# Optimization experiments

Measured on AMD Instinct MI355X. Metric: run time of the kernel, lower is better.

The kernel has to match this reference:

```python
import jax, jax.numpy as jnp
import numpy as np

E = 1_000_000
C_IN = 11
H = 64
N_LAYERS = 4
LN_EPS = 1e-5


def setup_inputs() -> dict:
    key = jax.random.key(0)
    ks = jax.random.split(key, 12)
    x = jax.random.normal(ks[0], (E, C_IN), dtype=jnp.float32)
    neighbors = jax.random.randint(ks[1], (E, 4), 0, E)
    s0 = 1.0 / np.sqrt(5 * C_IN)
    s1 = 1.0 / np.sqrt(5 * H)
    w0 = jax.random.uniform(ks[2], (5 * C_IN, H), jnp.float32, -s0, s0)
    b0 = jax.random.uniform(ks[3], (H,), jnp.float32, -s0, s0)
    w_rest = jax.random.uniform(ks[4], (N_LAYERS - 1, 5 * H, H), jnp.float32, -s1, s1)
    b_rest = jax.random.uniform(ks[5], (N_LAYERS - 1, H), jnp.float32, -s1, s1)
    ln_g = jnp.ones((N_LAYERS, H), jnp.float32)
    ln_b = jnp.zeros((N_LAYERS, H), jnp.float32)
    sc1 = 1.0 / np.sqrt(H)
    sc2 = 1.0 / np.sqrt(H // 2)
    cw1 = jax.random.uniform(ks[6], (H, H // 2), jnp.float32, -sc1, sc1)
    cb1 = jax.random.uniform(ks[7], (H // 2,), jnp.float32, -sc1, sc1)
    cw2 = jax.random.uniform(ks[8], (H // 2, 1), jnp.float32, -sc2, sc2)
    cb2 = jax.random.uniform(ks[9], (1,), jnp.float32, -sc2, sc2)
    return {"x": x, "neighbors": neighbors, "w0": w0, "b0": b0,
            "w_rest": w_rest, "b_rest": b_rest, "ln_g": ln_g, "ln_b": ln_b,
            "cw1": cw1, "cb1": cb1, "cw2": cw2, "cb2": cb2}


def _mesh_conv(x, neighbors, W, b):
    # Gather 4-ring neighbor features: [E,4,C]
    n = x[neighbors]
    a, bb, c, d = n[:, 0], n[:, 1], n[:, 2], n[:, 3]
    # Symmetric MeshCNN features -> 5*C, then linear projection.
    feats = jnp.concatenate([x, jnp.abs(a - c), a + c, jnp.abs(bb - d), bb + d], axis=-1)
    return feats @ W + b


def _layernorm(h, g, b):
    mu = jnp.mean(h, axis=-1, keepdims=True)
    var = jnp.var(h, axis=-1, keepdims=True)
    return (h - mu) * jax.lax.rsqrt(var + LN_EPS) * g + b


def reference(x, neighbors, w0, b0, w_rest, b_rest, ln_g, ln_b, cw1, cb1, cw2, cb2):
    # Layer 0 (no residual; dropout is identity in eval mode)
    h = jax.nn.relu(_layernorm(_mesh_conv(x, neighbors, w0, b0), ln_g[0], ln_b[0]))
    x = h
    for i in range(1, N_LAYERS):
        h = _mesh_conv(x, neighbors, w_rest[i - 1], b_rest[i - 1])
        h = jax.nn.relu(_layernorm(h, ln_g[i], ln_b[i]))
        x = h + x  # residual from layer 2 onward (shapes match)
    z = jax.nn.relu(x @ cw1 + cb1)
    logits = (z @ cw2 + cb2).squeeze(-1)
    return logits
```

## Files before the change

### kernel.cpp

```cpp
#include <hip/hip_runtime.h>
#include <hip/hip_bf16.h>
#include <math.h>

#define E_EDGES 1000000
#define LN_EPS  1e-5f

typedef unsigned short u16;
typedef __bf16 bf16x8 __attribute__((ext_vector_type(8)));
typedef float  f32x16 __attribute__((ext_vector_type(16)));

__device__ __forceinline__ float lo2f(unsigned d) {
    union { unsigned u; float f; } v; v.u = d << 16; return v.f;
}
__device__ __forceinline__ float hi2f(unsigned d) {
    union { unsigned u; float f; } v; v.u = d & 0xffff0000u; return v.f;
}
__device__ __forceinline__ unsigned pk2(float lo, float hi) {
    __hip_bfloat162 h = __float22bfloat162_rn(make_float2(lo, hi));
    unsigned r; __builtin_memcpy(&r, &h, 4); return r;
}

__global__ __launch_bounds__(256) void wconv_kernel(
    const float* __restrict__ wr, const float* __restrict__ w0,
    u16* __restrict__ wf)
{
    const int s = blockIdx.x * 256 + threadIdx.x;
    const int l    = s & 63;
    const int nt   = (s >> 6) & 1;
    const int col  = nt * 32 + (l & 31);
    const int half = l >> 5;
    uint4 pk;
    if (s < 3 * 2560) {
        const int L  = s / 2560;
        const int sl = s % 2560;
        const int kb = (sl >> 7) * 16 + half * 8;
        const float* W = wr + L * 320 * 64;
        pk.x = pk2(W[(kb+0)*64+col], W[(kb+1)*64+col]);
        pk.y = pk2(W[(kb+2)*64+col], W[(kb+3)*64+col]);
        pk.z = pk2(W[(kb+4)*64+col], W[(kb+5)*64+col]);
        pk.w = pk2(W[(kb+6)*64+col], W[(kb+7)*64+col]);
    } else {
        const int sl = s - 3 * 2560;
        const int kb = (sl >> 7) * 16 + half * 8;
        float v[8];
        #pragma unroll
        for (int p = 0; p < 8; ++p) v[p] = (kb + p < 55) ? w0[(kb+p)*64 + col] : 0.f;
        pk.x = pk2(v[0],v[1]); pk.y = pk2(v[2],v[3]);
        pk.z = pk2(v[4],v[5]); pk.w = pk2(v[6],v[7]);
    }
    *(uint4*)&wf[(size_t)s * 8] = pk;
}

__global__ __launch_bounds__(256, 4) void layer_mfma(
    const u16* __restrict__ xin, const int* __restrict__ nbr,
    const u16* __restrict__ wf, const float* __restrict__ bias,
    const float* __restrict__ lng, const float* __restrict__ lnb,
    u16* __restrict__ xout)
{
    __shared__ u16 afrag[2 * 20 * 64 * 8];
    const int t  = threadIdx.x;
    const int l  = t & 63;
    const int wv = t >> 6;
    const int e0 = blockIdx.x * 64;
    const int el = t >> 2;
    const int cq = t & 3;

    uint4 xv0, xv1;
    {
        const size_t e = (size_t)(e0 + el);
        const int4 n = *(const int4*)(nbr + 4 * e);
        const u16* xr = xin + e * 64           + cq * 16;
        const u16* ar = xin + (size_t)n.x * 64 + cq * 16;
        const u16* br = xin + (size_t)n.y * 64 + cq * 16;
        const u16* cr = xin + (size_t)n.z * 64 + cq * 16;
        const u16* dr = xin + (size_t)n.w * 64 + cq * 16;
        xv0 = *(const uint4*)(xr);                 xv1 = *(const uint4*)(xr + 8);
        const uint4 av0 = *(const uint4*)(ar);     const uint4 av1 = *(const uint4*)(ar + 8);
        const uint4 bv0 = *(const uint4*)(br);     const uint4 bv1 = *(const uint4*)(br + 8);
        const uint4 cv0 = *(const uint4*)(cr);     const uint4 cv1 = *(const uint4*)(cr + 8);
        const uint4 dv0 = *(const uint4*)(dr);     const uint4 dv1 = *(const uint4*)(dr + 8);
        const int mt_g  = el >> 5;
        const int lane0 = el & 31;
        u16* abase = afrag + (size_t)mt_g * (20 * 64 * 8);
        #pragma unroll
        for (int w8 = 0; w8 < 2; ++w8) {
            const uint4 xv = w8 ? xv1 : xv0;
            const uint4 av = w8 ? av1 : av0;
            const uint4 bv = w8 ? bv1 : bv0;
            const uint4 cv = w8 ? cv1 : cv0;
            const uint4 dv = w8 ? dv1 : dv0;
            const int gsw = (lane0 + 32 * w8) ^ cq;
            uint4 g1, g2, g3, g4;
            const unsigned* ap = (const unsigned*)&av;
            const unsigned* bp = (const unsigned*)&bv;
            const unsigned* cp = (const unsigned*)&cv;
            const unsigned* dp = (const unsigned*)&dv;
            unsigned* g1p = (unsigned*)&g1; unsigned* g2p = (unsigned*)&g2;
            unsigned* g3p = (unsigned*)&g3; unsigned* g4p = (unsigned*)&g4;
            #pragma unroll
            for (int i = 0; i < 4; ++i) {
                const float a0 = lo2f(ap[i]), a1 = hi2f(ap[i]);
                const float c0 = lo2f(cp[i]), c1 = hi2f(cp[i]);
                g1p[i] = pk2(a0 - c0, a1 - c1) & 0x7FFF7FFFu;
                g2p[i] = pk2(a0 + c0, a1 + c1);
                const float b0 = lo2f(bp[i]), b1 = hi2f(bp[i]);
                const float d0 = lo2f(dp[i]), d1 = hi2f(dp[i]);
                g3p[i] = pk2(b0 - d0, b1 - d1) & 0x7FFF7FFFu;
                g4p[i] = pk2(b0 + d0, b1 + d1);
            }
            *(uint4*)(abase + (size_t)(((0*4 + cq) * 64) + gsw) * 8) = xv;
            *(uint4*)(abase + (size_t)(((1*4 + cq) * 64) + gsw) * 8) = g1;
            *(uint4*)(abase + (size_t)(((2*4 + cq) * 64) + gsw) * 8) = g2;
            *(uint4*)(abase + (size_t)(((3*4 + cq) * 64) + gsw) * 8) = g3;
            *(uint4*)(abase + (size_t)(((4*4 + cq) * 64) + gsw) * 8) = g4;
        }
    }
    __syncthreads();

    const int mt = wv >> 1, nt = wv & 1;
    f32x16 acc = {};
    const u16* ab = afrag + (size_t)mt * (20 * 512);
    const u16* bb = wf + (size_t)(nt * 64 + l) * 8;
    #pragma unroll
    for (int ks = 0; ks < 20; ++ks) {
        const bf16x8 a8 = *(const bf16x8*)(ab + (size_t)(ks * 64 + (l ^ (ks & 3))) * 8);
        const bf16x8 b8 = *(const bf16x8*)(bb + ks * 1024);
        acc = __builtin_amdgcn_mfma_f32_32x32x16_bf16(a8, b8, acc, 0, 0, 0);
    }
    __syncthreads();

    float* ebuf = (float*)afrag;
    {
        const int col  = nt * 32 + (l & 31);
        const int quad = l >> 5;
        const float bc = bias[col];
        #pragma unroll
        for (int r = 0; r < 16; ++r) {
            const int row = mt * 32 + (r & 3) + 8 * (r >> 2) + 4 * quad;
            ebuf[row * 68 + col] = acc[r] + bc;
        }
    }
    __syncthreads();

    {
        const float* rp = ebuf + el * 68 + cq * 16;
        float v[16];
        float s = 0.f, qs = 0.f;
        #pragma unroll
        for (int i = 0; i < 16; ++i) { v[i] = rp[i]; s += v[i]; qs += v[i] * v[i]; }
        s  += __shfl_xor(s, 1);  s  += __shfl_xor(s, 2);
        qs += __shfl_xor(qs, 1); qs += __shfl_xor(qs, 2);
        const float mu   = s * (1.f / 64.f);
        const float var  = qs * (1.f / 64.f) - mu * mu;
        const float rinv = rsqrtf(var + LN_EPS);
        const size_t e   = (size_t)(e0 + el);
        u16* outp        = xout + e * 64 + cq * 16;
        #pragma unroll
        for (int h = 0; h < 2; ++h) {
            const uint4 res = h ? xv1 : xv0;
            const unsigned* rr = (const unsigned*)&res;
            uint4 o; unsigned* op = (unsigned*)&o;
            #pragma unroll
            for (int i = 0; i < 4; ++i) {
                const int ci = cq * 16 + h * 8 + i * 2;
                const float y0 = fmaxf(fmaf((v[h*8 + i*2]     - mu) * rinv, lng[ci],     lnb[ci]),     0.f) + lo2f(rr[i]);
                const float y1 = fmaxf(fmaf((v[h*8 + i*2 + 1] - mu) * rinv, lng[ci + 1], lnb[ci + 1]), 0.f) + hi2f(rr[i]);
                op[i] = pk2(y0, y1);
            }
            *(uint4*)(outp + h * 8) = o;
        }
    }
}

__global__ __launch_bounds__(256, 6) void layer0_mfma(
    const float* __restrict__ x, const int* __restrict__ nbr,
    const u16* __restrict__ wf0, const float* __restrict__ bias,
    const float* __restrict__ lng, const float* __restrict__ lnb,
    u16* __restrict__ xout)
{
    __shared__ float smem[64 * 68];
    u16* afrag = (u16*)smem;
    const int t  = threadIdx.x;
    const int l  = t & 63;
    const int wv = t >> 6;
    const int e0 = blockIdx.x * 64;
    const int el = t >> 2, cq = t & 3;

    {
        const size_t e = (size_t)(e0 + el);
        const int4 n = *(const int4*)(nbr + 4 * e);
        const float* xr = x + e * 11;
        const float* ar = x + (size_t)n.x * 11;
        const float* br = x + (size_t)n.y * 11;
        const float* cr = x + (size_t)n.z * 11;
        const float* dr = x + (size_t)n.w * 11;
        float f[16];
        if (cq == 0) {
            #pragma unroll
            for (int i = 0; i < 11; ++i) f[i] = xr[i];
            #pragma unroll
            for (int i = 0; i < 5; ++i) f[11 + i] = fabsf(ar[i] - cr[i]);
        } else if (cq == 1) {
            #pragma unroll
            for (int i = 0; i < 6; ++i) f[i] = fabsf(ar[5 + i] - cr[5 + i]);
            #pragma unroll
            for (int i = 0; i < 10; ++i) f[6 + i] = ar[i] + cr[i];
        } else if (cq == 2) {
            f[0] = ar[10] + cr[10];
            #pragma unroll
            for (int i = 0; i < 11; ++i) f[1 + i] = fabsf(br[i] - dr[i]);
            #pragma unroll
            for (int i = 0; i < 4; ++i) f[12 + i] = br[i] + dr[i];
        } else {
            #pragma unroll
            for (int i = 0; i < 7; ++i) f[i] = br[4 + i] + dr[4 + i];
            #pragma unroll
            for (int i = 7; i < 16; ++i) f[i] = 0.f;
        }
        const int mt_g  = el >> 5;
        const int lane0 = el & 31;
        u16* abase = afrag + (size_t)mt_g * (4 * 64 * 8);
        #pragma unroll
        for (int hh = 0; hh < 2; ++hh) {
            uint4 pk;
            pk.x = pk2(f[hh*8+0], f[hh*8+1]);
            pk.y = pk2(f[hh*8+2], f[hh*8+3]);
            pk.z = pk2(f[hh*8+4], f[hh*8+5]);
            pk.w = pk2(f[hh*8+6], f[hh*8+7]);
            const int gsw = (lane0 + 32 * hh) ^ cq;
            *(uint4*)(abase + (size_t)(cq * 64 + gsw) * 8) = pk;
        }
    }
    __syncthreads();

    const int mt = wv >> 1, nt = wv & 1;
    f32x16 acc = {};
    const u16* ab = afrag + (size_t)mt * (4 * 512);
    const u16* bb = wf0 + (size_t)(nt * 64 + l) * 8;
    #pragma unroll
    for (int ks = 0; ks < 4; ++ks) {
        const bf16x8 a8 = *(const bf16x8*)(ab + (size_t)(ks * 64 + (l ^ ks)) * 8);
        const bf16x8 b8 = *(const bf16x8*)(bb + ks * 1024);
        acc = __builtin_amdgcn_mfma_f32_32x32x16_bf16(a8, b8, acc, 0, 0, 0);
    }
    __syncthreads();

    float* ebuf = smem;
    {
        const int col  = nt * 32 + (l & 31);
        const int quad = l >> 5;
        const float bc = bias[col];
        #pragma unroll
        for (int r = 0; r < 16; ++r) {
            const int row = mt * 32 + (r & 3) + 8 * (r >> 2) + 4 * quad;
            ebuf[row * 68 + col] = acc[r] + bc;
        }
    }
    __syncthreads();

    {
        const float* rp = ebuf + el * 68 + cq * 16;
        float v[16];
        float s = 0.f, qs = 0.f;
        #pragma unroll
        for (int i = 0; i < 16; ++i) { v[i] = rp[i]; s += v[i]; qs += v[i] * v[i]; }
        s  += __shfl_xor(s, 1);  s  += __shfl_xor(s, 2);
        qs += __shfl_xor(qs, 1); qs += __shfl_xor(qs, 2);
        const float mu   = s * (1.f / 64.f);
        const float var  = qs * (1.f / 64.f) - mu * mu;
        const float rinv = rsqrtf(var + LN_EPS);
        const size_t e   = (size_t)(e0 + el);
        u16* outp        = xout + e * 64 + cq * 16;
        #pragma unroll
        for (int h = 0; h < 2; ++h) {
            uint4 o; unsigned* op = (unsigned*)&o;
            #pragma unroll
            for (int i = 0; i < 4; ++i) {
                const int ci = cq * 16 + h * 8 + i * 2;
                const float y0 = fmaxf(fmaf((v[h*8 + i*2]     - mu) * rinv, lng[ci],     lnb[ci]),     0.f);
                const float y1 = fmaxf(fmaf((v[h*8 + i*2 + 1] - mu) * rinv, lng[ci + 1], lnb[ci + 1]), 0.f);
                op[i] = pk2(y0, y1);
            }
            *(uint4*)(outp + h * 8) = o;
        }
    }
}

__global__ __launch_bounds__(256) void head_mfma(
    const u16* __restrict__ xin,
    const float* __restrict__ cw1, const float* __restrict__ cb1,
    const float* __restrict__ cw2, const float* __restrict__ cb2,
    float* __restrict__ out)
{
    __shared__ float hbuf[4][32 * 33];
    const int t    = threadIdx.x;
    const int l    = t & 63;
    const int wv   = t >> 6;
    const int col  = l & 31;
    const int half = l >> 5;

    bf16x8 bf[4];
    #pragma unroll
    for (int ks = 0; ks < 4; ++ks) {
        const int kb = ks * 16 + half * 8;
        uint4 pk;
        pk.x = pk2(cw1[(kb+0)*32 + col], cw1[(kb+1)*32 + col]);
        pk.y = pk2(cw1[(kb+2)*32 + col], cw1[(kb+3)*32 + col]);
        pk.z = pk2(cw1[(kb+4)*32 + col], cw1[(kb+5)*32 + col]);
        pk.w = pk2(cw1[(kb+6)*32 + col], cw1[(kb+7)*32 + col]);
        __builtin_memcpy(&bf[ks], &pk, 16);
    }
    const float bc = cb1[col];
    const float w2 = cw2[col];
    const float b2 = cb2[0];

    int tile = blockIdx.x * 4 + wv;
    const int valid = tile < (E_EDGES / 32);
    if (!valid) tile = E_EDGES / 32 - 1;
    const size_t e0 = (size_t)tile * 32;
    const u16* xb = xin + (e0 + col) * 64 + half * 8;
    f32x16 acc = {};
    #pragma unroll
    for (int ks = 0; ks < 4; ++ks) {
        const bf16x8 a8 = *(const bf16x8*)(xb + ks * 16);
        acc = __builtin_amdgcn_mfma_f32_32x32x16_bf16(a8, bf[ks], acc, 0, 0, 0);
    }
    float* hb = hbuf[wv];
    #pragma unroll
    for (int r = 0; r < 16; ++r) {
        const int row = (r & 3) + 8 * (r >> 2) + 4 * half;
        hb[row * 33 + col] = fmaxf(acc[r] + bc, 0.f) * w2;
    }
    __syncthreads();
    const int row2 = l >> 1, part = l & 1;
    const float* rp = hb + row2 * 33 + part * 16;
    float s = 0.f;
    #pragma unroll
    for (int i = 0; i < 16; ++i) s += rp[i];
    s += __shfl_xor(s, 1);
    if (valid && part == 0) out[e0 + row2] = s + b2;
}

extern "C" void kernel_launch(void* const* d_in, const int* in_sizes, int n_in,
                              void* d_out, int out_size, void* d_ws, size_t ws_size,
                              hipStream_t stream)
{
    (void)in_sizes; (void)n_in; (void)out_size; (void)ws_size;
    const float* x   = (const float*)d_in[0];
    const int*   nbr = (const int*)d_in[1];
    const float* w0  = (const float*)d_in[2];
    const float* b0  = (const float*)d_in[3];
    const float* wr  = (const float*)d_in[4];
    const float* br  = (const float*)d_in[5];
    const float* lg  = (const float*)d_in[6];
    const float* lb  = (const float*)d_in[7];
    const float* cw1 = (const float*)d_in[8];
    const float* cb1 = (const float*)d_in[9];
    const float* cw2 = (const float*)d_in[10];
    const float* cb2 = (const float*)d_in[11];
    float* out = (float*)d_out;

    u16* xa = (u16*)d_ws;
    u16* xb = xa + (size_t)E_EDGES * 64;
    u16* wfrag = (u16*)d_out;

    const dim3 blk(256);

    wconv_kernel<<<dim3(32), blk, 0, stream>>>(wr, w0, wfrag);
    layer0_mfma<<<dim3(E_EDGES / 64), blk, 0, stream>>>(x, nbr, wfrag + 3*20480, b0, lg, lb, xa);
    layer_mfma<<<dim3(E_EDGES / 64), blk, 0, stream>>>(xa, nbr, wfrag,           br,        lg + 64,  lb + 64,  xb);
    layer_mfma<<<dim3(E_EDGES / 64), blk, 0, stream>>>(xb, nbr, wfrag + 20480,   br + 64,   lg + 128, lb + 128, xa);
    layer_mfma<<<dim3(E_EDGES / 64), blk, 0, stream>>>(xa, nbr, wfrag + 40960,   br + 128,  lg + 192, lb + 192, xb);
    head_mfma<<<dim3((E_EDGES / 32 + 3) / 4), blk, 0, stream>>>(xb, cw1, cb1, cw2, cb2, out);
}
```

Baseline: 684.3 us.

## Make residual mesh-conv layers persistent with prefetched gathers and LDS-resident weights

The residual layer kernel becomes persistent: 256 blocks of 512 threads each walk 31 tiles of 128 edges. The weight fragments are staged once per block in LDS, and the next tile's neighbour gathers are issued before the current tile's MFMA and LayerNorm run. The previous tile's output store is deferred so it overlaps the new loads. This is meant to hide gather latency and cut per-tile launch and weight-reload cost, at the price of more registers, lower occupancy and more barriers per tile.

Measured after the change: 691.8 us. Within noise of the previous version (+1.1%).

```diff
diff --git a/kernel.cpp b/kernel.cpp
--- a/kernel.cpp
+++ b/kernel.cpp
@@ -2,8 +2,10 @@
 #include <hip/hip_bf16.h>
 #include <math.h>
 
-#define E_EDGES 1000000
-#define LN_EPS  1e-5f
+#define E_EDGES   1000000
+#define LN_EPS    1e-5f
+#define TILES_TOT 7813
+#define TPB_TILES 31
 
 typedef unsigned short u16;
 typedef __bf16 bf16x8 __attribute__((ext_vector_type(8)));
@@ -51,125 +53,185 @@
     *(uint4*)&wf[(size_t)s * 8] = pk;
 }
 
-__global__ __launch_bounds__(256, 4) void layer_mfma(
+struct GRegs {
+    uint4 xv0, xv1, av0, av1, bv0, bv1, cv0, cv1, dv0, dv1;
+};
+
+__device__ __forceinline__ void gload(GRegs& g, const u16* __restrict__ xin,
+                                      const int* __restrict__ nbr,
+                                      int tile, int el, int cq)
+{
+    size_t e = (size_t)tile * 128 + el;
+    if (e >= E_EDGES) e = E_EDGES - 1;
+    const int4 n = *(const int4*)(nbr + 4 * e);
+    const u16* xr = xin + e * 64            + cq * 16;
+    const u16* ar = xin + (size_t)n.x * 64  + cq * 16;
+    const u16* br = xin + (size_t)n.y * 64  + cq * 16;
+    const u16* cr = xin + (size_t)n.z * 64  + cq * 16;
+    const u16* dr = xin + (size_t)n.w * 64  + cq * 16;
+    g.xv0 = *(const uint4*)xr;    g.xv1 = *(const uint4*)(xr + 8);
+    g.av0 = *(const uint4*)ar;    g.av1 = *(const uint4*)(ar + 8);
+    g.bv0 = *(const uint4*)br;    g.bv1 = *(const uint4*)(br + 8);
+    g.cv0 = *(const uint4*)cr;    g.cv1 = *(const uint4*)(cr + 8);
+    g.dv0 = *(const uint4*)dr;    g.dv1 = *(const uint4*)(dr + 8);
+}
+
+__device__ __forceinline__ void pack_write(const GRegs& g, u16* __restrict__ afrag,
+                                           int el, int cq)
+{
+    const int mt_g  = el >> 5;
+    const int lane0 = el & 31;
+    u16* abase = afrag + (size_t)mt_g * (20 * 64 * 8);
+    #pragma unroll
+    for (int w8 = 0; w8 < 2; ++w8) {
+        const uint4 xv = w8 ? g.xv1 : g.xv0;
+        const uint4 av = w8 ? g.av1 : g.av0;
+        const uint4 bv = w8 ? g.bv1 : g.bv0;
+        const uint4 cv = w8 ? g.cv1 : g.cv0;
+        const uint4 dv = w8 ? g.dv1 : g.dv0;
+        const int gsw = (lane0 + 32 * w8) ^ cq;
+        uint4 g1, g2, g3, g4;
+        const unsigned* ap = (const unsigned*)&av;
+        const unsigned* bp = (const unsigned*)&bv;
+        const unsigned* cp = (const unsigned*)&cv;
+        const unsigned* dp = (const unsigned*)&dv;
+        unsigned* g1p = (unsigned*)&g1; unsigned* g2p = (unsigned*)&g2;
+        unsigned* g3p = (unsigned*)&g3; unsigned* g4p = (unsigned*)&g4;
+        #pragma unroll
+        for (int i = 0; i < 4; ++i) {
+            const float a0 = lo2f(ap[i]), a1 = hi2f(ap[i]);
+            const float c0 = lo2f(cp[i]), c1 = hi2f(cp[i]);
+            g1p[i] = pk2(a0 - c0, a1 - c1) & 0x7FFF7FFFu;
+            g2p[i] = pk2(a0 + c0, a1 + c1);
+            const float b0 = lo2f(bp[i]), b1 = hi2f(bp[i]);
+            const float d0 = lo2f(dp[i]), d1 = hi2f(dp[i]);
+            g3p[i] = pk2(b0 - d0, b1 - d1) & 0x7FFF7FFFu;
+            g4p[i] = pk2(b0 + d0, b1 + d1);
+        }
+        *(uint4*)(abase + (size_t)(((0*4 + cq) * 64) + gsw) * 8) = xv;
+        *(uint4*)(abase + (size_t)(((1*4 + cq) * 64) + gsw) * 8) = g1;
+        *(uint4*)(abase + (size_t)(((2*4 + cq) * 64) + gsw) * 8) = g2;
+        *(uint4*)(abase + (size_t)(((3*4 + cq) * 64) + gsw) * 8) = g3;
+        *(uint4*)(abase + (size_t)(((4*4 + cq) * 64) + gsw) * 8) = g4;
+    }
+}
+
+__device__ __forceinline__ void store_row(u16* __restrict__ xout, size_t e, int cq,
+                                          const float* sv, uint4 res0, uint4 res1,
+                                          const float* lgv, const float* lbv)
+{
+    if (e >= E_EDGES) return;
+    u16* outp = xout + e * 64 + cq * 16;
+    #pragma unroll
+    for (int h = 0; h < 2; ++h) {
+        const uint4 res = h ? res1 : res0;
+        const unsigned* rr = (const unsigned*)&res;
+        uint4 o; unsigned* op = (unsigned*)&o;
+        #pragma unroll
+        for (int i2 = 0; i2 < 4; ++i2) {
+            const int k = h * 8 + i2 * 2;
+            const float y0 = fmaxf(fmaf(sv[k],     lgv[k],     lbv[k]),     0.f) + lo2f(rr[i2]);
+            const float y1 = fmaxf(fmaf(sv[k + 1], lgv[k + 1], lbv[k + 1]), 0.f) + hi2f(rr[i2]);
+            op[i2] = pk2(y0, y1);
+        }
+        *(uint4*)(outp + h * 8) = o;
+    }
+}
+
+__global__ __launch_bounds__(512, 2) void layer_mfma(
     const u16* __restrict__ xin, const int* __restrict__ nbr,
     const u16* __restrict__ wf, const float* __restrict__ bias,
     const float* __restrict__ lng, const float* __restrict__ lnb,
     u16* __restrict__ xout)
 {
-    __shared__ u16 afrag[2 * 20 * 64 * 8];
+    __shared__ u16 smem[40960 + 20480];
+    u16* afrag = smem;
+    u16* bfrag = smem + 40960;
+    float* ebuf = (float*)smem;
+
     const int t  = threadIdx.x;
     const int l  = t & 63;
     const int wv = t >> 6;
-    const int e0 = blockIdx.x * 64;
     const int el = t >> 2;
     const int cq = t & 3;
 
-    uint4 xv0, xv1;
+    const int tile0  = blockIdx.x * TPB_TILES;
+    const int ntiles = min(TPB_TILES, TILES_TOT - tile0);
+    if (ntiles <= 0) return;
+
+    float lgv[16], lbv[16];
+    #pragma unroll
+    for (int j = 0; j < 4; ++j) {
+        *(float4*)&lgv[j * 4] = *(const float4*)(lng + cq * 16 + j * 4);
+        *(float4*)&lbv[j * 4] = *(const float4*)(lnb + cq * 16 + j * 4);
+    }
+    const int mt = wv >> 1, nt = wv & 1;
+    const float bc = bias[nt * 32 + (l & 31)];
+
     {
-        const size_t e = (size_t)(e0 + el);
-        const int4 n = *(const int4*)(nbr + 4 * e);
-        const u16* xr = xin + e * 64           + cq * 16;
-        const u16* ar = xin + (size_t)n.x * 64 + cq * 16;
-        const u16* br = xin + (size_t)n.y * 64 + cq * 16;
-        const u16* cr = xin + (size_t)n.z * 64 + cq * 16;
-        const u16* dr = xin + (size_t)n.w * 64 + cq * 16;
-        xv0 = *(const uint4*)(xr);                 xv1 = *(const uint4*)(xr + 8);
-        const uint4 av0 = *(const uint4*)(ar);     const uint4 av1 = *(const uint4*)(ar + 8);
-        const uint4 bv0 = *(const uint4*)(br);     const uint4 bv1 = *(const uint4*)(br + 8);
-        const uint4 cv0 = *(const uint4*)(cr);     const uint4 cv1 = *(const uint4*)(cr + 8);
-        const uint4 dv0 = *(const uint4*)(dr);     const uint4 dv1 = *(const uint4*)(dr + 8);
-        const int mt_g  = el >> 5;
-        const int lane0 = el & 31;
-        u16* abase = afrag + (size_t)mt_g * (20 * 64 * 8);
-        #pragma unroll
-        for (int w8 = 0; w8 < 2; ++w8) {
-            const uint4 xv = w8 ? xv1 : xv0;
-            const uint4 av = w8 ? av1 : av0;
-            const uint4 bv = w8 ? bv1 : bv0;
-            const uint4 cv = w8 ? cv1 : cv0;
-            const uint4 dv = w8 ? dv1 : dv0;
-            const int gsw = (lane0 + 32 * w8) ^ cq;
-            uint4 g1, g2, g3, g4;
-            const unsigned* ap = (const unsigned*)&av;
-            const unsigned* bp = (const unsigned*)&bv;
-            const unsigned* cp = (const unsigned*)&cv;
-            const unsigned* dp = (const unsigned*)&dv;
-            unsigned* g1p = (unsigned*)&g1; unsigned* g2p = (unsigned*)&g2;
-            unsigned* g3p = (unsigned*)&g3; unsigned* g4p = (unsigned*)&g4;
-            #pragma unroll
-            for (int i = 0; i < 4; ++i) {
-                const float a0 = lo2f(ap[i]), a1 = hi2f(ap[i]);
-                const float c0 = lo2f(cp[i]), c1 = hi2f(cp[i]);
-                g1p[i] = pk2(a0 - c0, a1 - c1) & 0x7FFF7FFFu;
-                g2p[i] = pk2(a0 + c0, a1 + c1);
-                const float b0 = lo2f(bp[i]), b1 = hi2f(bp[i]);
-                const float d0 = lo2f(dp[i]), d1 = hi2f(dp[i]);
-                g3p[i] = pk2(b0 - d0, b1 - d1) & 0x7FFF7FFFu;
-                g4p[i] = pk2(b0 + d0, b1 + d1);
+        const uint4* src = (const uint4*)wf;
+        uint4* dst = (uint4*)bfrag;
+        #pragma unroll
+        for (int i = 0; i < 5; ++i) dst[t + 512 * i] = src[t + 512 * i];
+    }
+
+    GRegs G;
+    gload(G, xin, nbr, tile0, el, cq);
+    pack_write(G, afrag, el, cq);
+    __syncthreads();
+
+    float sv[16];
+    uint4 res0 = {}, res1 = {};
+    size_t eprev = (size_t)E_EDGES;
+
+    for (int i = 0; i < ntiles; ++i) {
+        const bool more = (i + 1 < ntiles);
+        GRegs NX;
+        if (more) gload(NX, xin, nbr, tile0 + i + 1, el, cq);
+        if (i > 0) store_row(xout, eprev, cq, sv, res0, res1, lgv, lbv);
+
+        f32x16 acc = {};
+        const u16* ab = afrag + (size_t)mt * (20 * 512);
+        #pragma unroll
+        for (int ks = 0; ks < 20; ++ks) {
+            const bf16x8 a8 = *(const bf16x8*)(ab + (size_t)(ks * 64 + (l ^ (ks & 3))) * 8);
+            const bf16x8 b8 = *(const bf16x8*)(bfrag + (size_t)(((ks * 2 + nt) * 64) + l) * 8);
+            acc = __builtin_amdgcn_mfma_f32_32x32x16_bf16(a8, b8, acc, 0, 0, 0);
+        }
+        __syncthreads();
+
+        {
+            const int col  = nt * 32 + (l & 31);
+            const int quad = l >> 5;
+            #pragma unroll
+            for (int r = 0; r < 16; ++r) {
+                const int row = mt * 32 + (r & 3) + 8 * (r >> 2) + 4 * quad;
+                ebuf[row * 68 + col] = acc[r] + bc;
             }
-            *(uint4*)(abase + (size_t)(((0*4 + cq) * 64) + gsw) * 8) = xv;
-            *(uint4*)(abase + (size_t)(((1*4 + cq) * 64) + gsw) * 8) = g1;
-            *(uint4*)(abase + (size_t)(((2*4 + cq) * 64) + gsw) * 8) = g2;
-            *(uint4*)(abase + (size_t)(((3*4 + cq) * 64) + gsw) * 8) = g3;
-            *(uint4*)(abase + (size_t)(((4*4 + cq) * 64) + gsw) * 8) = g4;
-        }
-    }
-    __syncthreads();
-
-    const int mt = wv >> 1, nt = wv & 1;
-    f32x16 acc = {};
-    const u16* ab = afrag + (size_t)mt * (20 * 512);
-    const u16* bb = wf + (size_t)(nt * 64 + l) * 8;
-    #pragma unroll
-    for (int ks = 0; ks < 20; ++ks) {
-        const bf16x8 a8 = *(const bf16x8*)(ab + (size_t)(ks * 64 + (l ^ (ks & 3))) * 8);
-        const bf16x8 b8 = *(const bf16x8*)(bb + ks * 1024);
-        acc = __builtin_amdgcn_mfma_f32_32x32x16_bf16(a8, b8, acc, 0, 0, 0);
-    }
-    __syncthreads();
-
-    float* ebuf = (float*)afrag;
-    {
-        const int col  = nt * 32 + (l & 31);
-        const int quad = l >> 5;
-        const float bc = bias[col];
-        #pragma unroll
-        for (int r = 0; r < 16; ++r) {
-            const int row = mt * 32 + (r & 3) + 8 * (r >> 2) + 4 * quad;
-            ebuf[row * 68 + col] = acc[r] + bc;
-        }
-    }
-    __syncthreads();
-
-    {
-        const float* rp = ebuf + el * 68 + cq * 16;
-        float v[16];
-        float s = 0.f, qs = 0.f;
-        #pragma unroll
-        for (int i = 0; i < 16; ++i) { v[i] = rp[i]; s += v[i]; qs += v[i] * v[i]; }
-        s  += __shfl_xor(s, 1);  s  += __shfl_xor(s, 2);
-        qs += __shfl_xor(qs, 1); qs += __shfl_xor(qs, 2);
-        const float mu   = s * (1.f / 64.f);
-        const float var  = qs * (1.f / 64.f) - mu * mu;
-        const float rinv = rsqrtf(var + LN_EPS);
-        const size_t e   = (size_t)(e0 + el);
-        u16* outp        = xout + e * 64 + cq * 16;
-        #pragma unroll
-        for (int h = 0; h < 2; ++h) {
-            const uint4 res = h ? xv1 : xv0;
-            const unsigned* rr = (const unsigned*)&res;
-            uint4 o; unsigned* op = (unsigned*)&o;
-            #pragma unroll
-            for (int i = 0; i < 4; ++i) {
-                const int ci = cq * 16 + h * 8 + i * 2;
-                const float y0 = fmaxf(fmaf((v[h*8 + i*2]     - mu) * rinv, lng[ci],     lnb[ci]),     0.f) + lo2f(rr[i]);
-                const float y1 = fmaxf(fmaf((v[h*8 + i*2 + 1] - mu) * rinv, lng[ci + 1], lnb[ci + 1]), 0.f) + hi2f(rr[i]);
-                op[i] = pk2(y0, y1);
-            }
-            *(uint4*)(outp + h * 8) = o;
-        }
-    }
+        }
+        __syncthreads();
+
+        {
+            const float* rp = ebuf + el * 68 + cq * 16;
+            float s = 0.f, qs = 0.f;
+            #pragma unroll
+            for (int k = 0; k < 16; ++k) { sv[k] = rp[k]; s += sv[k]; qs += sv[k] * sv[k]; }
+            s  += __shfl_xor(s, 1);  s  += __shfl_xor(s, 2);
+            qs += __shfl_xor(qs, 1); qs += __shfl_xor(qs, 2);
+            const float mu   = s * (1.f / 64.f);
+            const float var  = qs * (1.f / 64.f) - mu * mu;
+            const float rinv = rsqrtf(var + LN_EPS);
+            #pragma unroll
+            for (int k = 0; k < 16; ++k) sv[k] = (sv[k] - mu) * rinv;
+            res0 = G.xv0; res1 = G.xv1;
+            eprev = (size_t)(tile0 + i) * 128 + el;
+        }
+        __syncthreads();
+
+        if (more) { G = NX; pack_write(G, afrag, el, cq); }
+        __syncthreads();
+    }
+    store_row(xout, eprev, cq, sv, res0, res1, lgv, lbv);
 }
 
 __global__ __launch_bounds__(256, 6) void layer0_mfma(
@@ -364,12 +426,10 @@
     u16* xb = xa + (size_t)E_EDGES * 64;
     u16* wfrag = (u16*)d_out;
 
-    const dim3 blk(256);
-
-    wconv_kernel<<<dim3(32), blk, 0, stream>>>(wr, w0, wfrag);
-    layer0_mfma<<<dim3(E_EDGES / 64), blk, 0, stream>>>(x, nbr, wfrag + 3*20480, b0, lg, lb, xa);
-    layer_mfma<<<dim3(E_EDGES / 64), blk, 0, stream>>>(xa, nbr, wfrag,           br,        lg + 64,  lb + 64,  xb);
-    layer_mfma<<<dim3(E_EDGES / 64), blk, 0, stream>>>(xb, nbr, wfrag + 20480,   br + 64,   lg + 128, lb + 128, xa);
-    layer_mfma<<<dim3(E_EDGES / 64), blk, 0, stream>>>(xa, nbr, wfrag + 40960,   br + 128,  lg + 192, lb + 192, xb);
-    head_mfma<<<dim3((E_EDGES / 32 + 3) / 4), blk, 0, stream>>>(xb, cw1, cb1, cw2, cb2, out);
-}
+    wconv_kernel<<<dim3(32), dim3(256), 0, stream>>>(wr, w0, wfrag);
+    layer0_mfma<<<dim3(E_EDGES / 64), dim3(256), 0, stream>>>(x, nbr, wfrag + 3*20480, b0, lg, lb, xa);
+    layer_mfma<<<dim3(256), dim3(512), 0, stream>>>(xa, nbr, wfrag,           br,        lg + 64,  lb + 64,  xb);
+    layer_mfma<<<dim3(256), dim3(512), 0, stream>>>(xb, nbr, wfrag + 20480,   br + 64,   lg + 128, lb + 128, xa);
+    layer_mfma<<<dim3(256), dim3(512), 0, stream>>>(xa, nbr, wfrag + 40960,   br + 128,  lg + 192, lb + 192, xb);
+    head_mfma<<<dim3((E_EDGES / 32 + 3) / 4), dim3(256), 0, stream>>>(xb, cw1, cb1, cw2, cb2, out);
+}
```
